# Optimization experiments

Hardware: AMD Instinct MI355X
Metric: run time of the kernel (lower is better)

Reference implementation:

```python
import jax, jax.numpy as jnp
import numpy as np

N = 10000   # num_nodes
U = 64      # num_units (rnn hidden per node)
DIN = 2     # input_dim per node
B = 16      # batch
E = 160000  # nnz of sparse support (avg degree 16)
D = DIN + U # concat feature size per node


def setup_inputs() -> dict:
    key = jax.random.key(0)
    ks = jax.random.split(key, 8)
    inputs = jax.random.normal(ks[0], (B, N * DIN), jnp.float32)
    hx = jax.random.normal(ks[1], (B, N * U), jnp.float32)
    # sparse support (scaled laplacian) in COO edge-list form
    rows = jax.random.randint(ks[2], (E,), 0, N, jnp.int32)
    cols = jax.random.randint(ks[3], (E,), 0, N, jnp.int32)
    vals = jax.random.normal(ks[4], (E,), jnp.float32) / 16.0
    # fc params: (input_size, 2*U), bias_start=1.0
    W_fc = jax.random.normal(ks[5], (D, 2 * U), jnp.float32) * (2.0 / (D + 2 * U)) ** 0.5
    b_fc = jnp.full((2 * U,), 1.0, jnp.float32)
    # gconv params: (input_size * num_matrices, U) with num_matrices = 2, bias_start=0.0
    W_g = jax.random.normal(ks[6], (2 * D, U), jnp.float32) * (2.0 / (2 * D + U)) ** 0.5
    b_g = jnp.zeros((U,), jnp.float32)
    return {"inputs": inputs, "hx": hx, "rows": rows, "cols": cols, "vals": vals,
            "W_fc": W_fc, "b_fc": b_fc, "W_g": W_g, "b_g": b_g}


def reference(inputs, hx, rows, cols, vals, W_fc, b_fc, W_g, b_g):
    # ---- gates via _fc (use_gc_for_ru=False), bias_start=1.0 ----
    xi = inputs.reshape(B * N, DIN)
    h = hx.reshape(B * N, U)
    cat = jnp.concatenate([xi, h], axis=-1)                  # (B*N, D)
    value = jax.nn.sigmoid(cat @ W_fc + b_fc)                # (B*N, 2U)
    value = value.reshape(B, N, 2 * U)
    r = value[..., :U].reshape(B, N * U)
    u = value[..., U:].reshape(B, N * U)

    # ---- candidate via _gconv(inputs, r*hx, U) ----
    xs = jnp.concatenate([inputs.reshape(B, N, DIN),
                          (r * hx).reshape(B, N, U)], axis=-1)  # (B, N, D)
    x0 = xs.transpose(1, 2, 0).reshape(N, D * B)             # (N, D*B)
    # sparse support matmul: x1 = S @ x0 via gather + segment_sum
    x1 = jax.ops.segment_sum(vals[:, None] * x0[cols], rows, num_segments=N)
    x = jnp.stack([x0, x1], axis=0)                          # (2, N, D*B)
    x = x.reshape(2, N, D, B).transpose(3, 1, 2, 0).reshape(B * N, D * 2)
    c = jnp.tanh(x @ W_g + b_g).reshape(B, N * U)            # activation = tanh

    # ---- GRU combine ----
    return u * hx + (1.0 - u) * c
```

## Files before the change

kernel.cpp:

```cpp
#include <hip/hip_runtime.h>

#define NN   10000
#define UU   64
#define DINP 2
#define BB   16
#define EE   160000
#define DCAT 66
#define XST  72
#define NPB  4
#define ECAP 64

typedef short short8 __attribute__((ext_vector_type(8)));
typedef float f32x4 __attribute__((ext_vector_type(4)));
typedef float f32x2 __attribute__((ext_vector_type(2)));

static __device__ __forceinline__ unsigned short f2bf(float f) {
  union { float f; unsigned u; } c; c.f = f;
  unsigned r = c.u + 0x7fffu + ((c.u >> 16) & 1u);
  return (unsigned short)(r >> 16);
}
static __device__ __forceinline__ float bf_lo(unsigned u) {
  union { unsigned u; float f; } c; c.u = u << 16; return c.f;
}
static __device__ __forceinline__ float bf_hi(unsigned u) {
  union { unsigned u; float f; } c; c.u = u & 0xffff0000u; return c.f;
}
static __device__ __forceinline__ float sigf(float x)   { return 1.0f / (1.0f + __expf(-x)); }
static __device__ __forceinline__ float tanh_f(float x) { return 2.0f / (1.0f + __expf(-2.0f * x)) - 1.0f; }

__global__ void k_scatter(const int* __restrict__ rows, const int* __restrict__ cols,
                          const float* __restrict__ vals, int* __restrict__ cnt,
                          int2* __restrict__ edges) {
  int e = blockIdx.x * 256 + threadIdx.x;
  if (e >= EE) return;
  int r = rows[e];
  int p = atomicAdd(&cnt[r], 1);
  if (p < ECAP) {
    union { float f; int i; } v; v.f = vals[e];
    edges[r * ECAP + p] = make_int2(cols[e], v.i);
  }
}

__global__ __launch_bounds__(256) void k1_gates_cand(
    const float* __restrict__ inp, const float* __restrict__ hx,
    const float* __restrict__ Wfc, const float* __restrict__ bfc_g,
    const float* __restrict__ Wg, const float* __restrict__ bg,
    unsigned* __restrict__ pack, unsigned* __restrict__ z8) {
  __shared__ unsigned short xsl[2][16 * XST];

  const int tid = threadIdx.x;
  const int w = tid >> 6;
  const int lane = tid & 63;
  const int lr = lane & 15;
  const int lg = lane >> 4;
  const int jr = w * 16 + lr;

  const float bfc0 = bfc_g[jr];
  const float bfc1 = bfc_g[64 + jr];
  const float bgv  = bg[jr];

  short8 ffc0[3], ffc1[3], fg0r[3], fg1r[3];
#pragma unroll
  for (int c = 0; c < 3; ++c) {
#pragma unroll
    for (int e = 0; e < 8; ++e) {
      int k = c * 32 + lg * 8 + e;
      float v0 = 0.f, v1 = 0.f, g0 = 0.f, g1 = 0.f;
      if (k < 64) {
        v0 = Wfc[(k + 2) * 128 + jr];
        v1 = Wfc[(k + 2) * 128 + 64 + jr];
        g0 = Wg[(2 * k + 4) * 64 + jr];
        g1 = Wg[(2 * k + 5) * 64 + jr];
      } else if (k < 66) {
        int kk = k - 64;
        v0 = Wfc[kk * 128 + jr];
        v1 = Wfc[kk * 128 + 64 + jr];
        g0 = Wg[(2 * kk) * 64 + jr];
        g1 = Wg[(2 * kk + 1) * 64 + jr];
      }
      ffc0[c][e] = (short)f2bf(v0); ffc1[c][e] = (short)f2bf(v1);
      fg0r[c][e] = (short)f2bf(g0); fg1r[c][e] = (short)f2bf(g1);
    }
  }

  const int n0 = blockIdx.x * NPB;
  const float* hrow = hx + (size_t)lr * (NN * UU);
  const float* irow = inp + (size_t)lr * (NN * DINP);

  float4 h0, h1, h2, h3; float2 xf = {0.f, 0.f}; float hj[4];
  {
    const float* hp = hrow + (size_t)n0 * UU;
    h0 = *(const float4*)&hp[lg * 8];      h1 = *(const float4*)&hp[lg * 8 + 4];
    h2 = *(const float4*)&hp[32 + lg * 8]; h3 = *(const float4*)&hp[32 + lg * 8 + 4];
    if (lg == 0) xf = *(const float2*)&irow[(size_t)n0 * DINP];
#pragma unroll
    for (int reg = 0; reg < 4; ++reg)
      hj[reg] = hx[(size_t)(lg * 4 + reg) * (NN * UU) + (size_t)n0 * UU + jr];
  }

  for (int i = 0; i < NPB; ++i) {
    const int n = n0 + i;
    unsigned short* xb = &xsl[i & 1][0];

    short8 a0, a1, a2;
    a0[0] = (short)f2bf(h0.x); a0[1] = (short)f2bf(h0.y);
    a0[2] = (short)f2bf(h0.z); a0[3] = (short)f2bf(h0.w);
    a0[4] = (short)f2bf(h1.x); a0[5] = (short)f2bf(h1.y);
    a0[6] = (short)f2bf(h1.z); a0[7] = (short)f2bf(h1.w);
    a1[0] = (short)f2bf(h2.x); a1[1] = (short)f2bf(h2.y);
    a1[2] = (short)f2bf(h2.z); a1[3] = (short)f2bf(h2.w);
    a1[4] = (short)f2bf(h3.x); a1[5] = (short)f2bf(h3.y);
    a1[6] = (short)f2bf(h3.z); a1[7] = (short)f2bf(h3.w);
    a2 = (short8){0, 0, 0, 0, 0, 0, 0, 0};
    a2[0] = (short)f2bf(xf.x); a2[1] = (short)f2bf(xf.y);

    f32x4 accr = {0.f, 0.f, 0.f, 0.f}, accu = {0.f, 0.f, 0.f, 0.f};
    accr = __builtin_amdgcn_mfma_f32_16x16x32_bf16(a0, ffc0[0], accr, 0, 0, 0);
    accu = __builtin_amdgcn_mfma_f32_16x16x32_bf16(a0, ffc1[0], accu, 0, 0, 0);
    accr = __builtin_amdgcn_mfma_f32_16x16x32_bf16(a1, ffc0[1], accr, 0, 0, 0);
    accu = __builtin_amdgcn_mfma_f32_16x16x32_bf16(a1, ffc1[1], accu, 0, 0, 0);
    accr = __builtin_amdgcn_mfma_f32_16x16x32_bf16(a2, ffc0[2], accr, 0, 0, 0);
    accu = __builtin_amdgcn_mfma_f32_16x16x32_bf16(a2, ffc1[2], accu, 0, 0, 0);

    float4 nh0 = h0, nh1 = h1, nh2 = h2, nh3 = h3;
    float2 nxf = xf; float nhj[4];
#pragma unroll
    for (int reg = 0; reg < 4; ++reg) nhj[reg] = hj[reg];
    if (i + 1 < NPB) {
      const int n2 = n + 1;
      const float* hp = hrow + (size_t)n2 * UU;
      nh0 = *(const float4*)&hp[lg * 8];      nh1 = *(const float4*)&hp[lg * 8 + 4];
      nh2 = *(const float4*)&hp[32 + lg * 8]; nh3 = *(const float4*)&hp[32 + lg * 8 + 4];
      if (lg == 0) nxf = *(const float2*)&irow[(size_t)n2 * DINP];
#pragma unroll
      for (int reg = 0; reg < 4; ++reg)
        nhj[reg] = hx[(size_t)(lg * 4 + reg) * (NN * UU) + (size_t)n2 * UU + jr];
    }

    unsigned ub[4];
#pragma unroll
    for (int reg = 0; reg < 4; ++reg) {
      int b = lg * 4 + reg;
      float r = sigf(accr[reg] + bfc0);
      xb[b * XST + jr] = f2bf(r * hj[reg]);
      ub[reg] = (unsigned)f2bf(sigf(accu[reg] + bfc1));
    }
    __syncthreads();

    short8 x0v = *(const short8*)&xb[lr * XST + lg * 8];
    short8 x1v = *(const short8*)&xb[lr * XST + 32 + lg * 8];
    f32x4 accy = {0.f, 0.f, 0.f, 0.f}, accz = {0.f, 0.f, 0.f, 0.f};
    accy = __builtin_amdgcn_mfma_f32_16x16x32_bf16(x0v, fg0r[0], accy, 0, 0, 0);
    accz = __builtin_amdgcn_mfma_f32_16x16x32_bf16(x0v, fg1r[0], accz, 0, 0, 0);
    accy = __builtin_amdgcn_mfma_f32_16x16x32_bf16(x1v, fg0r[1], accy, 0, 0, 0);
    accz = __builtin_amdgcn_mfma_f32_16x16x32_bf16(x1v, fg1r[1], accz, 0, 0, 0);
    accy = __builtin_amdgcn_mfma_f32_16x16x32_bf16(a2,  fg0r[2], accy, 0, 0, 0);
    accz = __builtin_amdgcn_mfma_f32_16x16x32_bf16(a2,  fg1r[2], accz, 0, 0, 0);

#pragma unroll
    for (int reg = 0; reg < 4; ++reg) {
      int b = lg * 4 + reg;
      pack[b * (NN * UU) + n * UU + jr] =
          (((unsigned)f2bf(accy[reg] + bgv)) << 16) | ub[reg];
    }
    unsigned zw = (unsigned)__builtin_amdgcn_cvt_pk_fp8_f32(accz[0], accz[1], 0, 0);
    zw = (unsigned)__builtin_amdgcn_cvt_pk_fp8_f32(accz[2], accz[3], (int)zw, 1);
    z8[n * 256 + w * 64 + lg * 16 + lr] = zw;

    h0 = nh0; h1 = nh1; h2 = nh2; h3 = nh3; xf = nxf;
#pragma unroll
    for (int reg = 0; reg < 4; ++reg) hj[reg] = nhj[reg];
  }
}

static __device__ __forceinline__ void load_edge(int i, int deg, const int2* ep,
                                                 const unsigned* zl,
                                                 uint4& z, float& v) {
  int ii = (i < deg) ? i : (deg - 1);
  int2 e = ep[ii];
  int col = __builtin_amdgcn_readfirstlane(e.x);
  int vb  = __builtin_amdgcn_readfirstlane(e.y);
  union { int i; float f; } cv; cv.i = vb;
  v = (i < deg) ? cv.f : 0.f;
  z = *(const uint4*)(zl + (size_t)col * 256);
}

static __device__ __forceinline__ void consume_edge(uint4 z, float v,
                                                    float (&acc)[4][4]) {
  unsigned zw[4] = {z.x, z.y, z.z, z.w};
#pragma unroll
  for (int q = 0; q < 4; ++q) {
    f32x2 lo = __builtin_amdgcn_cvt_pk_f32_fp8((int)zw[q], 0);
    f32x2 hi = __builtin_amdgcn_cvt_pk_f32_fp8((int)zw[q], 1);
    acc[q][0] += v * lo[0]; acc[q][1] += v * lo[1];
    acc[q][2] += v * hi[0]; acc[q][3] += v * hi[1];
  }
}

static __device__ __forceinline__ uint4 combine4(uint4 pk, float4 hv,
                                                 float a0, float a1,
                                                 float a2, float a3) {
  float aa[4] = {a0, a1, a2, a3};
  unsigned pkk[4] = {pk.x, pk.y, pk.z, pk.w};
  float hh[4] = {hv.x, hv.y, hv.z, hv.w};
  unsigned ov[4];
#pragma unroll
  for (int q = 0; q < 4; ++q) {
    float u = bf_lo(pkk[q]);
    float c = tanh_f(bf_hi(pkk[q]) + aa[q]);
    union { float f; unsigned u; } o;
    o.f = u * hh[q] + (1.f - u) * c;
    ov[q] = o.u;
  }
  return (uint4){ov[0], ov[1], ov[2], ov[3]};
}

__global__ __launch_bounds__(256) void k2_agg_combine(
    const int* __restrict__ cnt, const int2* __restrict__ edges,
    const unsigned* __restrict__ z8, const float* __restrict__ hx,
    unsigned* __restrict__ pack) {
  const int lane = threadIdx.x & 63;
  const int n = blockIdx.x * 4 + (threadIdx.x >> 6);
  const int jw = lane >> 4;
  const int lg = (lane >> 2) & 3;
  const int ja = lane & 3;
  const int jb = jw * 16 + ja * 4;

  const size_t f0 = (size_t)(lg * 4 + 0) * (NN * UU) + (size_t)n * UU + jb;
  const size_t f1 = f0 + (size_t)(NN * UU);
  const size_t f2 = f1 + (size_t)(NN * UU);
  const size_t f3 = f2 + (size_t)(NN * UU);
  uint4 pk0 = *(const uint4*)&pack[f0]; float4 hv0 = *(const float4*)&hx[f0];
  uint4 pk1 = *(const uint4*)&pack[f1]; float4 hv1 = *(const float4*)&hx[f1];
  uint4 pk2 = *(const uint4*)&pack[f2]; float4 hv2 = *(const float4*)&hx[f2];
  uint4 pk3 = *(const uint4*)&pack[f3]; float4 hv3 = *(const float4*)&hx[f3];

  float acc[4][4];
#pragma unroll
  for (int q = 0; q < 4; ++q)
#pragma unroll
    for (int m = 0; m < 4; ++m) acc[q][m] = 0.f;

  int deg = cnt[n];
  deg = (deg < ECAP) ? deg : ECAP;
  const int2* ep = edges + n * ECAP;
  const unsigned* zl = z8 + (size_t)lane * 4;

  if (deg > 0) {
    uint4 zA, zB, zC, zD; float vA, vB, vC, vD;
    load_edge(0, deg, ep, zl, zA, vA);
    load_edge(1, deg, ep, zl, zB, vB);
    load_edge(2, deg, ep, zl, zC, vC);
    load_edge(3, deg, ep, zl, zD, vD);
    for (int s = 0; s < deg; s += 4) {
      uint4 zE, zF, zG, zH; float vE, vF, vG, vH;
      load_edge(s + 4, deg, ep, zl, zE, vE);
      load_edge(s + 5, deg, ep, zl, zF, vF);
      load_edge(s + 6, deg, ep, zl, zG, vG);
      load_edge(s + 7, deg, ep, zl, zH, vH);
      consume_edge(zA, vA, acc);
      consume_edge(zB, vB, acc);
      consume_edge(zC, vC, acc);
      consume_edge(zD, vD, acc);
      zA = zE; vA = vE; zB = zF; vB = vF;
      zC = zG; vC = vG; zD = zH; vD = vH;
    }
  }

  *(uint4*)&pack[f0] = combine4(pk0, hv0, acc[0][0], acc[1][0], acc[2][0], acc[3][0]);
  *(uint4*)&pack[f1] = combine4(pk1, hv1, acc[0][1], acc[1][1], acc[2][1], acc[3][1]);
  *(uint4*)&pack[f2] = combine4(pk2, hv2, acc[0][2], acc[1][2], acc[2][2], acc[3][2]);
  *(uint4*)&pack[f3] = combine4(pk3, hv3, acc[0][3], acc[1][3], acc[2][3], acc[3][3]);
}

extern "C" void kernel_launch(void* const* d_in, const int* in_sizes, int n_in,
                              void* d_out, int out_size, void* d_ws, size_t ws_size,
                              hipStream_t stream) {
  const float* inp  = (const float*)d_in[0];
  const float* hx   = (const float*)d_in[1];
  const int*   rows = (const int*)d_in[2];
  const int*   cols = (const int*)d_in[3];
  const float* vals = (const float*)d_in[4];
  const float* Wfc  = (const float*)d_in[5];
  const float* bfc  = (const float*)d_in[6];
  const float* Wg   = (const float*)d_in[7];
  const float* bg   = (const float*)d_in[8];
  unsigned* pack = (unsigned*)d_out;

  char* ws = (char*)d_ws;
  unsigned* z8  = (unsigned*)(ws + 0);
  int*  cnt     = (int*)(ws + 10240000);
  int2* edges   = (int2*)(ws + 10280064);

  hipMemsetAsync(cnt, 0, NN * sizeof(int), stream);
  k_scatter<<<(EE + 255) / 256, 256, 0, stream>>>(rows, cols, vals, cnt, edges);
  k1_gates_cand<<<NN / NPB, 256, 0, stream>>>(inp, hx, Wfc, bfc, Wg, bg, pack, z8);
  k2_agg_combine<<<NN / 4, 256, 0, stream>>>(cnt, edges, z8, hx, pack);
}
```

Measured before the change: 195.9 us.

## Split node edge lists across two waves and swizzle candidate LDS tile

```diff
diff --git a/kernel.cpp b/kernel.cpp
--- a/kernel.cpp
+++ b/kernel.cpp
@@ -1,12 +1,11 @@
 #include <hip/hip_runtime.h>
+#include <hip/hip_bf16.h>
 
 #define NN   10000
 #define UU   64
 #define DINP 2
 #define BB   16
 #define EE   160000
-#define DCAT 66
-#define XST  72
 #define NPB  4
 #define ECAP 64
 
@@ -18,6 +17,11 @@
   union { float f; unsigned u; } c; c.f = f;
   unsigned r = c.u + 0x7fffu + ((c.u >> 16) & 1u);
   return (unsigned short)(r >> 16);
+}
+static __device__ __forceinline__ unsigned cvtpk_bf16(float a, float b) {
+  union { __hip_bfloat162 h; unsigned u; } c;
+  c.h = __float22bfloat162_rn(make_float2(a, b));
+  return c.u;
 }
 static __device__ __forceinline__ float bf_lo(unsigned u) {
   union { unsigned u; float f; } c; c.u = u << 16; return c.f;
@@ -46,7 +50,7 @@
     const float* __restrict__ Wfc, const float* __restrict__ bfc_g,
     const float* __restrict__ Wg, const float* __restrict__ bg,
     unsigned* __restrict__ pack, unsigned* __restrict__ z8) {
-  __shared__ unsigned short xsl[2][16 * XST];
+  __shared__ unsigned short xsl[2][16 * 64];
 
   const int tid = threadIdx.x;
   const int w = tid >> 6;
@@ -100,19 +104,16 @@
 
   for (int i = 0; i < NPB; ++i) {
     const int n = n0 + i;
-    unsigned short* xb = &xsl[i & 1][0];
-
-    short8 a0, a1, a2;
-    a0[0] = (short)f2bf(h0.x); a0[1] = (short)f2bf(h0.y);
-    a0[2] = (short)f2bf(h0.z); a0[3] = (short)f2bf(h0.w);
-    a0[4] = (short)f2bf(h1.x); a0[5] = (short)f2bf(h1.y);
-    a0[6] = (short)f2bf(h1.z); a0[7] = (short)f2bf(h1.w);
-    a1[0] = (short)f2bf(h2.x); a1[1] = (short)f2bf(h2.y);
-    a1[2] = (short)f2bf(h2.z); a1[3] = (short)f2bf(h2.w);
-    a1[4] = (short)f2bf(h3.x); a1[5] = (short)f2bf(h3.y);
-    a1[6] = (short)f2bf(h3.z); a1[7] = (short)f2bf(h3.w);
-    a2 = (short8){0, 0, 0, 0, 0, 0, 0, 0};
-    a2[0] = (short)f2bf(xf.x); a2[1] = (short)f2bf(xf.y);
+    char* xb = (char*)&xsl[i & 1][0];
+
+    union { int4 i4; short8 s8; } ua0, ua1, ua2;
+    ua0.i4.x = (int)cvtpk_bf16(h0.x, h0.y); ua0.i4.y = (int)cvtpk_bf16(h0.z, h0.w);
+    ua0.i4.z = (int)cvtpk_bf16(h1.x, h1.y); ua0.i4.w = (int)cvtpk_bf16(h1.z, h1.w);
+    ua1.i4.x = (int)cvtpk_bf16(h2.x, h2.y); ua1.i4.y = (int)cvtpk_bf16(h2.z, h2.w);
+    ua1.i4.z = (int)cvtpk_bf16(h3.x, h3.y); ua1.i4.w = (int)cvtpk_bf16(h3.z, h3.w);
+    ua2.i4 = (int4){0, 0, 0, 0};
+    ua2.i4.x = (int)cvtpk_bf16(xf.x, xf.y);
+    short8 a0 = ua0.s8, a1 = ua1.s8, a2 = ua2.s8;
 
     f32x4 accr = {0.f, 0.f, 0.f, 0.f}, accu = {0.f, 0.f, 0.f, 0.f};
     accr = __builtin_amdgcn_mfma_f32_16x16x32_bf16(a0, ffc0[0], accr, 0, 0, 0);
@@ -137,18 +138,26 @@
         nhj[reg] = hx[(size_t)(lg * 4 + reg) * (NN * UU) + (size_t)n2 * UU + jr];
     }
 
-    unsigned ub[4];
-#pragma unroll
-    for (int reg = 0; reg < 4; ++reg) {
-      int b = lg * 4 + reg;
-      float r = sigf(accr[reg] + bfc0);
-      xb[b * XST + jr] = f2bf(r * hj[reg]);
-      ub[reg] = (unsigned)f2bf(sigf(accu[reg] + bfc1));
+    float uf[4];
+    {
+      float rh0 = sigf(accr[0] + bfc0) * hj[0];
+      float rh1 = sigf(accr[1] + bfc0) * hj[1];
+      float rh2 = sigf(accr[2] + bfc0) * hj[2];
+      float rh3 = sigf(accr[3] + bfc0) * hj[3];
+      unsigned p01 = cvtpk_bf16(rh0, rh1);
+      unsigned p23 = cvtpk_bf16(rh2, rh3);
+      const int b0 = lg * 4;
+      *(unsigned short*)(xb + ((( b0      * 128) + jr * 2) ^ (( b0      & 7) << 4))) = (unsigned short)p01;
+      *(unsigned short*)(xb + ((((b0 + 1) * 128) + jr * 2) ^ (((b0 + 1) & 7) << 4))) = (unsigned short)(p01 >> 16);
+      *(unsigned short*)(xb + ((((b0 + 2) * 128) + jr * 2) ^ (((b0 + 2) & 7) << 4))) = (unsigned short)p23;
+      *(unsigned short*)(xb + ((((b0 + 3) * 128) + jr * 2) ^ (((b0 + 3) & 7) << 4))) = (unsigned short)(p23 >> 16);
+      uf[0] = sigf(accu[0] + bfc1); uf[1] = sigf(accu[1] + bfc1);
+      uf[2] = sigf(accu[2] + bfc1); uf[3] = sigf(accu[3] + bfc1);
     }
     __syncthreads();
 
-    short8 x0v = *(const short8*)&xb[lr * XST + lg * 8];
-    short8 x1v = *(const short8*)&xb[lr * XST + 32 + lg * 8];
+    short8 x0v = *(const short8*)(xb + ((lr * 128 + lg * 16)       ^ ((lr & 7) << 4)));
+    short8 x1v = *(const short8*)(xb + ((lr * 128 + (4 + lg) * 16) ^ ((lr & 7) << 4)));
     f32x4 accy = {0.f, 0.f, 0.f, 0.f}, accz = {0.f, 0.f, 0.f, 0.f};
     accy = __builtin_amdgcn_mfma_f32_16x16x32_bf16(x0v, fg0r[0], accy, 0, 0, 0);
     accz = __builtin_amdgcn_mfma_f32_16x16x32_bf16(x0v, fg1r[0], accz, 0, 0, 0);
@@ -160,8 +169,7 @@
 #pragma unroll
     for (int reg = 0; reg < 4; ++reg) {
       int b = lg * 4 + reg;
-      pack[b * (NN * UU) + n * UU + jr] =
-          (((unsigned)f2bf(accy[reg] + bgv)) << 16) | ub[reg];
+      pack[b * (NN * UU) + n * UU + jr] = cvtpk_bf16(uf[reg], accy[reg] + bgv);
     }
     unsigned zw = (unsigned)__builtin_amdgcn_cvt_pk_fp8_f32(accz[0], accz[1], 0, 0);
     zw = (unsigned)__builtin_amdgcn_cvt_pk_fp8_f32(accz[2], accz[3], (int)zw, 1);
@@ -173,15 +181,17 @@
   }
 }
 
-static __device__ __forceinline__ void load_edge(int i, int deg, const int2* ep,
-                                                 const unsigned* zl,
+static __device__ __forceinline__ void load_edge(int i, int myc, int half, int deg,
+                                                 const int2* ep, const unsigned* zl,
                                                  uint4& z, float& v) {
-  int ii = (i < deg) ? i : (deg - 1);
-  int2 e = ep[ii];
+  int ii = (i < myc) ? i : (myc - 1);
+  int p = half + 2 * ii;
+  p = (p < deg) ? p : 0;
+  int2 e = ep[p];
   int col = __builtin_amdgcn_readfirstlane(e.x);
   int vb  = __builtin_amdgcn_readfirstlane(e.y);
   union { int i; float f; } cv; cv.i = vb;
-  v = (i < deg) ? cv.f : 0.f;
+  v = (i < myc) ? cv.f : 0.f;
   z = *(const uint4*)(zl + (size_t)col * 256);
 }
 
@@ -219,8 +229,12 @@
     const int* __restrict__ cnt, const int2* __restrict__ edges,
     const unsigned* __restrict__ z8, const float* __restrict__ hx,
     unsigned* __restrict__ pack) {
+  __shared__ float sacc[2][64 * 17];
   const int lane = threadIdx.x & 63;
-  const int n = blockIdx.x * 4 + (threadIdx.x >> 6);
+  const int w = threadIdx.x >> 6;
+  const int nh = w >> 1;
+  const int half = w & 1;
+  const int n = blockIdx.x * 2 + nh;
   const int jw = lane >> 4;
   const int lg = (lane >> 2) & 3;
   const int ja = lane & 3;
@@ -230,10 +244,13 @@
   const size_t f1 = f0 + (size_t)(NN * UU);
   const size_t f2 = f1 + (size_t)(NN * UU);
   const size_t f3 = f2 + (size_t)(NN * UU);
-  uint4 pk0 = *(const uint4*)&pack[f0]; float4 hv0 = *(const float4*)&hx[f0];
-  uint4 pk1 = *(const uint4*)&pack[f1]; float4 hv1 = *(const float4*)&hx[f1];
-  uint4 pk2 = *(const uint4*)&pack[f2]; float4 hv2 = *(const float4*)&hx[f2];
-  uint4 pk3 = *(const uint4*)&pack[f3]; float4 hv3 = *(const float4*)&hx[f3];
+  uint4 pk0, pk1, pk2, pk3; float4 hv0, hv1, hv2, hv3;
+  if (half == 0) {
+    pk0 = *(const uint4*)&pack[f0]; hv0 = *(const float4*)&hx[f0];
+    pk1 = *(const uint4*)&pack[f1]; hv1 = *(const float4*)&hx[f1];
+    pk2 = *(const uint4*)&pack[f2]; hv2 = *(const float4*)&hx[f2];
+    pk3 = *(const uint4*)&pack[f3]; hv3 = *(const float4*)&hx[f3];
+  }
 
   float acc[4][4];
 #pragma unroll
@@ -243,21 +260,22 @@
 
   int deg = cnt[n];
   deg = (deg < ECAP) ? deg : ECAP;
+  const int myc = (deg > half) ? ((deg - half + 1) >> 1) : 0;
   const int2* ep = edges + n * ECAP;
   const unsigned* zl = z8 + (size_t)lane * 4;
 
-  if (deg > 0) {
+  if (myc > 0) {
     uint4 zA, zB, zC, zD; float vA, vB, vC, vD;
-    load_edge(0, deg, ep, zl, zA, vA);
-    load_edge(1, deg, ep, zl, zB, vB);
-    load_edge(2, deg, ep, zl, zC, vC);
-    load_edge(3, deg, ep, zl, zD, vD);
-    for (int s = 0; s < deg; s += 4) {
+    load_edge(0, myc, half, deg, ep, zl, zA, vA);
+    load_edge(1, myc, half, deg, ep, zl, zB, vB);
+    load_edge(2, myc, half, deg, ep, zl, zC, vC);
+    load_edge(3, myc, half, deg, ep, zl, zD, vD);
+    for (int s = 0; s < myc; s += 4) {
       uint4 zE, zF, zG, zH; float vE, vF, vG, vH;
-      load_edge(s + 4, deg, ep, zl, zE, vE);
-      load_edge(s + 5, deg, ep, zl, zF, vF);
-      load_edge(s + 6, deg, ep, zl, zG, vG);
-      load_edge(s + 7, deg, ep, zl, zH, vH);
+      load_edge(s + 4, myc, half, deg, ep, zl, zE, vE);
+      load_edge(s + 5, myc, half, deg, ep, zl, zF, vF);
+      load_edge(s + 6, myc, half, deg, ep, zl, zG, vG);
+      load_edge(s + 7, myc, half, deg, ep, zl, zH, vH);
       consume_edge(zA, vA, acc);
       consume_edge(zB, vB, acc);
       consume_edge(zC, vC, acc);
@@ -267,10 +285,26 @@
     }
   }
 
-  *(uint4*)&pack[f0] = combine4(pk0, hv0, acc[0][0], acc[1][0], acc[2][0], acc[3][0]);
-  *(uint4*)&pack[f1] = combine4(pk1, hv1, acc[0][1], acc[1][1], acc[2][1], acc[3][1]);
-  *(uint4*)&pack[f2] = combine4(pk2, hv2, acc[0][2], acc[1][2], acc[2][2], acc[3][2]);
-  *(uint4*)&pack[f3] = combine4(pk3, hv3, acc[0][3], acc[1][3], acc[2][3], acc[3][3]);
+  if (half == 1) {
+#pragma unroll
+    for (int q = 0; q < 4; ++q)
+#pragma unroll
+      for (int m = 0; m < 4; ++m)
+        sacc[nh][lane * 17 + q * 4 + m] = acc[q][m];
+  }
+  __syncthreads();
+  if (half == 0) {
+#pragma unroll
+    for (int q = 0; q < 4; ++q)
+#pragma unroll
+      for (int m = 0; m < 4; ++m)
+        acc[q][m] += sacc[nh][lane * 17 + q * 4 + m];
+
+    *(uint4*)&pack[f0] = combine4(pk0, hv0, acc[0][0], acc[1][0], acc[2][0], acc[3][0]);
+    *(uint4*)&pack[f1] = combine4(pk1, hv1, acc[0][1], acc[1][1], acc[2][1], acc[3][1]);
+    *(uint4*)&pack[f2] = combine4(pk2, hv2, acc[0][2], acc[1][2], acc[2][2], acc[3][2]);
+    *(uint4*)&pack[f3] = combine4(pk3, hv3, acc[0][3], acc[1][3], acc[2][3], acc[3][3]);
+  }
 }
 
 extern "C" void kernel_launch(void* const* d_in, const int* in_sizes, int n_in,
@@ -295,5 +329,5 @@
   hipMemsetAsync(cnt, 0, NN * sizeof(int), stream);
   k_scatter<<<(EE + 255) / 256, 256, 0, stream>>>(rows, cols, vals, cnt, edges);
   k1_gates_cand<<<NN / NPB, 256, 0, stream>>>(inp, hx, Wfc, bfc, Wg, bg, pack, z8);
-  k2_agg_combine<<<NN / 4, 256, 0, stream>>>(cnt, edges, z8, hx, pack);
-}
+  k2_agg_combine<<<NN / 2, 256, 0, stream>>>(cnt, edges, z8, hx, pack);
+}
```

Result: no change. 195.8 us (-0.0%).
